# Performance work log

Measured on AMD Instinct MI355X. Metric: run time of the kernel, lower is better.

## Reference

```python
import jax, jax.numpy as jnp
import numpy as np

B, C, H, W = 4, 512, 64, 64
C8 = C // 8


def setup_inputs() -> dict:
    key = jax.random.key(0)
    ks = jax.random.split(key, 8)
    return {
        "x": jax.random.normal(ks[0], (B, C, H, W), jnp.float32),
        "wb": jax.random.normal(ks[1], (C8, C), jnp.float32) * 0.05,
        "bb": jax.random.normal(ks[2], (C8,), jnp.float32) * 0.05,
        "wc": jax.random.normal(ks[3], (C8, C), jnp.float32) * 0.05,
        "bc": jax.random.normal(ks[4], (C8,), jnp.float32) * 0.05,
        "wd": jax.random.normal(ks[5], (C, C), jnp.float32) * 0.05,
        "bd": jax.random.normal(ks[6], (C,), jnp.float32) * 0.05,
        "alpha": jax.random.normal(ks[7], (1,), jnp.float32),
    }


def reference(x, wb, bb, wc, bc, wd, bd, alpha):
    b, c, h, w = x.shape
    n = h * w
    xf = x.reshape(b, c, n)  # [B, C, N]
    # 1x1 convs == per-pixel channel matmuls
    feat_b = jnp.einsum('kc,bcn->bkn', wb, xf) + bb[:, None]  # [B, C/8, N]
    feat_c = jnp.einsum('kc,bcn->bkn', wc, xf) + bc[:, None]  # [B, C/8, N]
    # attention_s[n, m] = softmax_m( feat_b[:, n] . feat_c[:, m] )  (no scaling, as in source)
    scores = jnp.einsum('bkn,bkm->bnm', feat_b, feat_c)  # [B, N, N]
    attn = jax.nn.softmax(scores, axis=-1)
    feat_d = jnp.einsum('oc,bcn->bon', wd, xf) + bd[:, None]  # [B, C, N]
    # feat_e = bmm(feat_d, attn^T): fe[c, n] = sum_m fd[c, m] * attn[n, m]
    feat_e = jnp.einsum('bcm,bnm->bcn', feat_d, attn).reshape(b, c, h, w)
    return alpha[0] * feat_e + x
```

## Files before the change

### kernel.cpp

```cpp
#include <hip/hip_runtime.h>
#include <hip/hip_bf16.h>

#define NB 4
#define CC 512
#define CK 64
#define NN 4096

typedef unsigned short u16;
typedef __attribute__((ext_vector_type(8))) __bf16 bf16x8;
typedef __attribute__((ext_vector_type(4))) float f32x4;
typedef __attribute__((ext_vector_type(4))) unsigned int u32x4;
typedef __attribute__((ext_vector_type(8))) unsigned short u16x8;
typedef __attribute__((ext_vector_type(4))) unsigned short u16x4;

__device__ __forceinline__ u16 f2b(float f) {
  union { float f; unsigned u; } x; x.f = f;
  unsigned r = x.u + 0x7fffu + ((x.u >> 16) & 1u);
  return (u16)(r >> 16);
}
__device__ __forceinline__ float b2f(u16 u) {
  union { unsigned u; float f; } x; x.u = ((unsigned)u) << 16; return x.f;
}

#define MFMA16(a, b, c) __builtin_amdgcn_mfma_f32_16x16x32_bf16((a), (b), (c), 0, 0, 0)

__global__ __launch_bounds__(256) void proj_qk(
    const float* __restrict__ x,
    const float* __restrict__ wb, const float* __restrict__ bb,
    const float* __restrict__ wc, const float* __restrict__ bc,
    u16* __restrict__ Qhi, u16* __restrict__ Qlo,
    u16* __restrict__ Khi, u16* __restrict__ Klo)
{
  const int tid = threadIdx.x;
  const int n0 = blockIdx.x * 64;
  const int which = blockIdx.y;
  const int b = blockIdx.z;
  const float* w   = which ? wc : wb;
  const float* bia = which ? bc : bb;
  u16* oh = which ? Khi : Qhi;
  u16* ol = which ? Klo : Qlo;

  __shared__ u16 Wh[64][40], Wl[64][40], Xh[64][40], Xl[64][40];

  const int lane = tid & 63, wid = tid >> 6;
  const int wr = wid >> 1, wn = wid & 1;
  const int l15 = lane & 15, lk = (lane >> 4) * 8;

  f32x4 acc[2][2] = {};

  for (int kk = 0; kk < CC; kk += 32) {
    {
      const int row = tid >> 2, c0 = (tid & 3) * 8;
      const float* src = w + (size_t)row * CC + kk + c0;
#pragma unroll
      for (int i = 0; i < 8; ++i) {
        float v = src[i];
        u16 h = f2b(v);
        Wh[row][c0 + i] = h;
        Wl[row][c0 + i] = f2b(v - b2f(h));
      }
    }
    {
      const int cc2 = tid >> 3, j0 = (tid & 7) * 8;
      const float* src = x + ((size_t)b * CC + kk + cc2) * NN + n0 + j0;
#pragma unroll
      for (int i = 0; i < 8; ++i) {
        float v = src[i];
        u16 h = f2b(v);
        Xh[j0 + i][cc2] = h;
        Xl[j0 + i][cc2] = f2b(v - b2f(h));
      }
    }
    __syncthreads();
#pragma unroll
    for (int fi = 0; fi < 2; ++fi) {
      const int ar = wr * 32 + fi * 16 + l15;
      bf16x8 ah = *(const bf16x8*)&Wh[ar][lk];
      bf16x8 al = *(const bf16x8*)&Wl[ar][lk];
#pragma unroll
      for (int fj = 0; fj < 2; ++fj) {
        const int br = wn * 32 + fj * 16 + l15;
        bf16x8 bh = *(const bf16x8*)&Xh[br][lk];
        bf16x8 bl = *(const bf16x8*)&Xl[br][lk];
        acc[fi][fj] = MFMA16(ah, bh, acc[fi][fj]);
        acc[fi][fj] = MFMA16(ah, bl, acc[fi][fj]);
        acc[fi][fj] = MFMA16(al, bh, acc[fi][fj]);
      }
    }
    __syncthreads();
  }

#pragma unroll
  for (int fi = 0; fi < 2; ++fi) {
    const int d0 = wr * 32 + fi * 16 + (lane >> 4) * 4;
#pragma unroll
    for (int fj = 0; fj < 2; ++fj) {
      const int n = n0 + wn * 32 + fj * 16 + l15;
      u16x4 vh, vl;
#pragma unroll
      for (int r = 0; r < 4; ++r) {
        float v = acc[fi][fj][r] + bia[d0 + r];
        u16 h = f2b(v);
        vh[r] = h;
        vl[r] = f2b(v - b2f(h));
      }
      *(u16x4*)&oh[((size_t)b * NN + n) * CK + d0] = vh;
      *(u16x4*)&ol[((size_t)b * NN + n) * CK + d0] = vl;
    }
  }
}

__global__ __launch_bounds__(256) void proj_v(
    const float* __restrict__ x,
    const float* __restrict__ wd, const float* __restrict__ bd,
    u16* __restrict__ Vt)
{
  const int tid = threadIdx.x;
  const int n0 = blockIdx.x * 64;
  const int o0 = blockIdx.y * 64;
  const int b = blockIdx.z;

  __shared__ u16 Wt[64][40], Xt[64][40];
  const int lane = tid & 63, wid = tid >> 6;
  const int wr = wid >> 1, wn = wid & 1;
  const int l15 = lane & 15, lk = (lane >> 4) * 8;

  f32x4 acc[2][2] = {};
  for (int kk = 0; kk < CC; kk += 32) {
    {
      const int row = tid >> 2, c0 = (tid & 3) * 8;
      const float* src = wd + (size_t)(o0 + row) * CC + kk + c0;
#pragma unroll
      for (int i = 0; i < 8; ++i) Wt[row][c0 + i] = f2b(src[i]);
    }
    {
      const int cc2 = tid >> 3, j0 = (tid & 7) * 8;
      const float* src = x + ((size_t)b * CC + kk + cc2) * NN + n0 + j0;
#pragma unroll
      for (int i = 0; i < 8; ++i) Xt[j0 + i][cc2] = f2b(src[i]);
    }
    __syncthreads();
#pragma unroll
    for (int fi = 0; fi < 2; ++fi) {
      bf16x8 a = *(const bf16x8*)&Wt[wr * 32 + fi * 16 + l15][lk];
#pragma unroll
      for (int fj = 0; fj < 2; ++fj) {
        bf16x8 bv = *(const bf16x8*)&Xt[wn * 32 + fj * 16 + l15][lk];
        acc[fi][fj] = MFMA16(a, bv, acc[fi][fj]);
      }
    }
    __syncthreads();
  }
#pragma unroll
  for (int fi = 0; fi < 2; ++fi) {
    const int d0 = o0 + wr * 32 + fi * 16 + (lane >> 4) * 4;
#pragma unroll
    for (int fj = 0; fj < 2; ++fj) {
      const int n = n0 + wn * 32 + fj * 16 + l15;
#pragma unroll
      for (int r = 0; r < 4; ++r)
        Vt[((size_t)b * CC + d0 + r) * NN + n] = f2b(acc[fi][fj][r] + bd[d0 + r]);
    }
  }
}

struct alignas(16) AttnLds {
  u16 kh[2][64][64];
  u16 kl[2][64][64];
  float s[64][68];
  u16 p[64][64];
  float m[64];
  float l[64];
  float sc[64];
};

__global__ __launch_bounds__(256, 2) void attn(
    const u16* __restrict__ Qhi, const u16* __restrict__ Qlo,
    const u16* __restrict__ Khi, const u16* __restrict__ Klo,
    const u16* __restrict__ Vt,
    const float* __restrict__ x, const float* __restrict__ alpha,
    float* __restrict__ out)
{
  __shared__ AttnLds L;
  const int tid = threadIdx.x;
  const int lane = tid & 63, wid = tid >> 6;
  const int bid = blockIdx.x;
  const int b = (bid >> 1) & 3;
  const int qt = bid >> 3;
  const int ohalf = bid & 1;
  const int q0 = qt * 64;
  const int l15 = lane & 15;
  const int lk8 = (lane >> 4) * 8;

  const int srow = tid >> 2;
  const int sch  = (tid & 3) * 16;
  const int ssw0 = sch ^ ((srow & 7) << 3);
  const int ssw1 = (sch + 8) ^ ((srow & 7) << 3);

  bf16x8 qah[2], qal[2];
  {
    const size_t qg = ((size_t)b * NN + q0 + wid * 16 + l15) * CK + lk8;
    qah[0] = *(const bf16x8*)&Qhi[qg];
    qah[1] = *(const bf16x8*)&Qhi[qg + 32];
    qal[0] = *(const bf16x8*)&Qlo[qg];
    qal[1] = *(const bf16x8*)&Qlo[qg + 32];
  }
  {
    const size_t g = ((size_t)b * NN + srow) * CK + sch;
    *(u32x4*)&L.kh[0][srow][ssw0] = *(const u32x4*)&Khi[g];
    *(u32x4*)&L.kh[0][srow][ssw1] = *(const u32x4*)&Khi[g + 8];
    *(u32x4*)&L.kl[0][srow][ssw0] = *(const u32x4*)&Klo[g];
    *(u32x4*)&L.kl[0][srow][ssw1] = *(const u32x4*)&Klo[g + 8];
  }
  if (tid < 64) { L.m[tid] = -__builtin_huge_valf(); L.l[tid] = 0.f; }

  const u16* vbase = Vt + ((size_t)b * CC + ohalf * 256 + wid * 64 + l15) * NN + lk8;

  f32x4 accO[4][4] = {};

  __syncthreads();

  for (int t = 0; t < 64; ++t) {
    const int m0 = t * 64;
    const int cur = t & 1;
    const bool hasNext = (t < 63);

    u32x4 kh0, kh1, kl0, kl1;
    if (hasNext) {
      const size_t g = ((size_t)b * NN + m0 + 64 + srow) * CK + sch;
      kh0 = *(const u32x4*)&Khi[g];
      kh1 = *(const u32x4*)&Khi[g + 8];
      kl0 = *(const u32x4*)&Klo[g];
      kl1 = *(const u32x4*)&Klo[g + 8];
    }
    bf16x8 vr[2][4];
#pragma unroll
    for (int f_ = 0; f_ < 4; ++f_)
#pragma unroll
      for (int ks = 0; ks < 2; ++ks)
        vr[ks][f_] = *(const bf16x8*)(vbase + (size_t)f_ * 16 * NN + m0 + ks * 32);

    __builtin_amdgcn_s_setprio(1);
#pragma unroll
    for (int fj = 0; fj < 4; ++fj) {
      f32x4 s = {};
#pragma unroll
      for (int ks = 0; ks < 2; ++ks) {
        const int k = ks * 32 + lk8;
        const int br = fj * 16 + l15;
        bf16x8 bh = *(const bf16x8*)&L.kh[cur][br][k ^ ((br & 7) << 3)];
        bf16x8 bl = *(const bf16x8*)&L.kl[cur][br][k ^ ((br & 7) << 3)];
        s = MFMA16(qah[ks], bh, s);
        s = MFMA16(qah[ks], bl, s);
        s = MFMA16(qal[ks], bh, s);
      }
      const int r0 = wid * 16 + (lane >> 4) * 4, c0 = fj * 16 + l15;
#pragma unroll
      for (int r = 0; r < 4; ++r) L.s[r0 + r][c0] = s[r];
    }
    __builtin_amdgcn_s_setprio(0);
    __syncthreads();

    if (hasNext) {
      *(u32x4*)&L.kh[cur ^ 1][srow][ssw0] = kh0;
      *(u32x4*)&L.kh[cur ^ 1][srow][ssw1] = kh1;
      *(u32x4*)&L.kl[cur ^ 1][srow][ssw0] = kl0;
      *(u32x4*)&L.kl[cur ^ 1][srow][ssw1] = kl1;
    }
    {
      const int row = srow, sub = tid & 3;
      const float* sr = &L.s[row][sch];
      f32x4 a0 = *(const f32x4*)&sr[0];
      f32x4 a1 = *(const f32x4*)&sr[4];
      f32x4 a2 = *(const f32x4*)&sr[8];
      f32x4 a3 = *(const f32x4*)&sr[12];
      float mx = fmaxf(fmaxf(fmaxf(a0[0], a0[1]), fmaxf(a0[2], a0[3])),
                       fmaxf(fmaxf(a1[0], a1[1]), fmaxf(a1[2], a1[3])));
      mx = fmaxf(mx, fmaxf(fmaxf(fmaxf(a2[0], a2[1]), fmaxf(a2[2], a2[3])),
                           fmaxf(fmaxf(a3[0], a3[1]), fmaxf(a3[2], a3[3]))));
      mx = fmaxf(mx, __shfl_xor(mx, 1));
      mx = fmaxf(mx, __shfl_xor(mx, 2));
      const float mOld = L.m[row];
      const float mNew = fmaxf(mOld, mx);
      float pv[16];
      float sum = 0.f;
#pragma unroll
      for (int j = 0; j < 4; ++j) { pv[j]      = __expf(a0[j] - mNew); sum += pv[j]; }
#pragma unroll
      for (int j = 0; j < 4; ++j) { pv[4 + j]  = __expf(a1[j] - mNew); sum += pv[4 + j]; }
#pragma unroll
      for (int j = 0; j < 4; ++j) { pv[8 + j]  = __expf(a2[j] - mNew); sum += pv[8 + j]; }
#pragma unroll
      for (int j = 0; j < 4; ++j) { pv[12 + j] = __expf(a3[j] - mNew); sum += pv[12 + j]; }
      sum += __shfl_xor(sum, 1);
      sum += __shfl_xor(sum, 2);
      const float scf = __expf(mOld - mNew);
      if (sub == 0) {
        L.m[row] = mNew;
        L.l[row] = L.l[row] * scf + sum;
        L.sc[row] = scf;
      }
      u16x8 pb0, pb1;
#pragma unroll
      for (int j = 0; j < 8; ++j) pb0[j] = f2b(pv[j]);
#pragma unroll
      for (int j = 0; j < 8; ++j) pb1[j] = f2b(pv[8 + j]);
      *(u16x8*)&L.p[row][ssw0] = pb0;
      *(u16x8*)&L.p[row][ssw1] = pb1;
    }
    __syncthreads();

#pragma unroll
    for (int f_ = 0; f_ < 4; ++f_) {
      const int r0 = f_ * 16 + (lane >> 4) * 4;
      float s0 = L.sc[r0], s1 = L.sc[r0 + 1], s2 = L.sc[r0 + 2], s3 = L.sc[r0 + 3];
#pragma unroll
      for (int fj = 0; fj < 4; ++fj) {
        accO[f_][fj][0] *= s0; accO[f_][fj][1] *= s1;
        accO[f_][fj][2] *= s2; accO[f_][fj][3] *= s3;
      }
    }
    __builtin_amdgcn_s_setprio(1);
#pragma unroll
    for (int ks = 0; ks < 2; ++ks) {
      const int k = ks * 32 + lk8;
      bf16x8 a[4];
#pragma unroll
      for (int f_ = 0; f_ < 4; ++f_) {
        const int ar = f_ * 16 + l15;
        a[f_] = *(const bf16x8*)&L.p[ar][k ^ ((ar & 7) << 3)];
      }
#pragma unroll
      for (int fj = 0; fj < 4; ++fj)
#pragma unroll
        for (int f_ = 0; f_ < 4; ++f_)
          accO[f_][fj] = MFMA16(a[f_], vr[ks][fj], accO[f_][fj]);
    }
    __builtin_amdgcn_s_setprio(0);
  }
  __syncthreads();
  const float al = alpha[0];
#pragma unroll
  for (int f_ = 0; f_ < 4; ++f_) {
    const int r0 = f_ * 16 + (lane >> 4) * 4;
    const float rl0 = 1.f / L.l[r0],     rl1 = 1.f / L.l[r0 + 1];
    const float rl2 = 1.f / L.l[r0 + 2], rl3 = 1.f / L.l[r0 + 3];
    const int n_ = q0 + r0;
#pragma unroll
    for (int fj = 0; fj < 4; ++fj) {
      const int c_ = ohalf * 256 + wid * 64 + fj * 16 + l15;
      const size_t g = ((size_t)b * CC + c_) * NN + n_;
      f32x4 xv = *(const f32x4*)&x[g];
      f32x4 ov;
      ov[0] = fmaf(al, accO[f_][fj][0] * rl0, xv[0]);
      ov[1] = fmaf(al, accO[f_][fj][1] * rl1, xv[1]);
      ov[2] = fmaf(al, accO[f_][fj][2] * rl2, xv[2]);
      ov[3] = fmaf(al, accO[f_][fj][3] * rl3, xv[3]);
      *(f32x4*)&out[g] = ov;
    }
  }
}

extern "C" void kernel_launch(void* const* d_in, const int* in_sizes, int n_in,
                              void* d_out, int out_size, void* d_ws, size_t ws_size,
                              hipStream_t stream) {
  const float* x     = (const float*)d_in[0];
  const float* wb    = (const float*)d_in[1];
  const float* bb    = (const float*)d_in[2];
  const float* wc    = (const float*)d_in[3];
  const float* bc    = (const float*)d_in[4];
  const float* wd    = (const float*)d_in[5];
  const float* bd    = (const float*)d_in[6];
  const float* alpha = (const float*)d_in[7];
  float* out = (float*)d_out;

  u16* Qhi = (u16*)d_ws;
  u16* Qlo = Qhi + (size_t)NB * NN * CK;
  u16* Khi = Qlo + (size_t)NB * NN * CK;
  u16* Klo = Khi + (size_t)NB * NN * CK;
  u16* Vt  = Klo + (size_t)NB * NN * CK;

  proj_qk<<<dim3(NN / 64, 2, NB), 256, 0, stream>>>(x, wb, bb, wc, bc, Qhi, Qlo, Khi, Klo);
  proj_v<<<dim3(NN / 64, CC / 64, NB), 256, 0, stream>>>(x, wd, bd, Vt);
  attn<<<dim3(512), 256, 0, stream>>>(Qhi, Qlo, Khi, Klo, Vt, x, alpha, out);
}
```

Before: 233.8 us.

## Retile attention to 32-query blocks covering all channels, with exp2 and lazy rescale

The attention kernel now gives each block 32 queries and all 512 output channels, instead of 64 queries and half the channels. This stops recomputing QK scores and softmax twice per query tile, at the cost of streaming all of V for each block. Q is pre-scaled by log2(e) in the projection so the softmax can use exp2f. The running max is only raised when it grows by more than a threshold, and the accumulator rescale is skipped when no row changed. The rescale threshold allows unnormalized exponents up to about 2^11.5, which risks precision loss in bf16 P, and the V loads are split around the score computation.

New measurement: 346.7 us. +48.3%, slower.

```diff
diff --git a/kernel.cpp b/kernel.cpp
--- a/kernel.cpp
+++ b/kernel.cpp
@@ -20,6 +20,9 @@
 }
 __device__ __forceinline__ float b2f(u16 u) {
   union { unsigned u; float f; } x; x.u = ((unsigned)u) << 16; return x.f;
+}
+__device__ __forceinline__ u16 cvt_bf16(float f) {
+  union { __bf16 h; u16 u; } c; c.h = (__bf16)f; return c.u;
 }
 
 #define MFMA16(a, b, c) __builtin_amdgcn_mfma_f32_16x16x32_bf16((a), (b), (c), 0, 0, 0)
@@ -39,6 +42,7 @@
   const float* bia = which ? bc : bb;
   u16* oh = which ? Khi : Qhi;
   u16* ol = which ? Klo : Qlo;
+  const float qsc = which ? 1.0f : 1.44269504088896340736f;
 
   __shared__ u16 Wh[64][40], Wl[64][40], Xh[64][40], Xl[64][40];
 
@@ -99,7 +103,7 @@
       u16x4 vh, vl;
 #pragma unroll
       for (int r = 0; r < 4; ++r) {
-        float v = acc[fi][fj][r] + bia[d0 + r];
+        float v = (acc[fi][fj][r] + bia[d0 + r]) * qsc;
         u16 h = f2b(v);
         vh[r] = h;
         vl[r] = f2b(v - b2f(h));
@@ -167,11 +171,11 @@
 struct alignas(16) AttnLds {
   u16 kh[2][64][64];
   u16 kl[2][64][64];
-  float s[64][68];
-  u16 p[64][64];
-  float m[64];
-  float l[64];
-  float sc[64];
+  float s[32][68];
+  u16 p[32][64];
+  float m[32];
+  float l[32];
+  float sc[32];
 };
 
 __global__ __launch_bounds__(256, 2) void attn(
@@ -186,20 +190,25 @@
   const int lane = tid & 63, wid = tid >> 6;
   const int bid = blockIdx.x;
   const int b = (bid >> 1) & 3;
-  const int qt = bid >> 3;
-  const int ohalf = bid & 1;
-  const int q0 = qt * 64;
+  const int qt = ((bid >> 3) << 1) | (bid & 1);
+  const int q0 = qt * 32;
   const int l15 = lane & 15;
   const int lk8 = (lane >> 4) * 8;
+
+  const int fi = wid >> 1;
+  const int fj0 = (wid & 1) * 2;
 
   const int srow = tid >> 2;
   const int sch  = (tid & 3) * 16;
   const int ssw0 = sch ^ ((srow & 7) << 3);
   const int ssw1 = (sch + 8) ^ ((srow & 7) << 3);
 
+  const int xrow = tid >> 3, xsub = tid & 7;
+  const int xsw = (xsub * 8) ^ ((xrow & 7) << 3);
+
   bf16x8 qah[2], qal[2];
   {
-    const size_t qg = ((size_t)b * NN + q0 + wid * 16 + l15) * CK + lk8;
+    const size_t qg = ((size_t)b * NN + q0 + fi * 16 + l15) * CK + lk8;
     qah[0] = *(const bf16x8*)&Qhi[qg];
     qah[1] = *(const bf16x8*)&Qhi[qg + 32];
     qal[0] = *(const bf16x8*)&Qlo[qg];
@@ -212,11 +221,11 @@
     *(u32x4*)&L.kl[0][srow][ssw0] = *(const u32x4*)&Klo[g];
     *(u32x4*)&L.kl[0][srow][ssw1] = *(const u32x4*)&Klo[g + 8];
   }
-  if (tid < 64) { L.m[tid] = -__builtin_huge_valf(); L.l[tid] = 0.f; }
-
-  const u16* vbase = Vt + ((size_t)b * CC + ohalf * 256 + wid * 64 + l15) * NN + lk8;
-
-  f32x4 accO[4][4] = {};
+  if (tid < 32) { L.m[tid] = -__builtin_huge_valf(); L.l[tid] = 0.f; }
+
+  const u16* vbase = Vt + ((size_t)b * CC + wid * 128 + l15) * NN + lk8;
+
+  f32x4 accO[2][8] = {};
 
   __syncthreads();
 
@@ -233,16 +242,15 @@
       kl0 = *(const u32x4*)&Klo[g];
       kl1 = *(const u32x4*)&Klo[g + 8];
     }
-    bf16x8 vr[2][4];
-#pragma unroll
-    for (int f_ = 0; f_ < 4; ++f_)
-#pragma unroll
-      for (int ks = 0; ks < 2; ++ks)
-        vr[ks][f_] = *(const bf16x8*)(vbase + (size_t)f_ * 16 * NN + m0 + ks * 32);
+    bf16x8 vr0[8], vr1[8];
+#pragma unroll
+    for (int f_ = 0; f_ < 8; ++f_)
+      vr0[f_] = *(const bf16x8*)(vbase + (size_t)f_ * 16 * NN + m0);
 
     __builtin_amdgcn_s_setprio(1);
 #pragma unroll
-    for (int fj = 0; fj < 4; ++fj) {
+    for (int f2 = 0; f2 < 2; ++f2) {
+      const int fj = fj0 + f2;
       f32x4 s = {};
 #pragma unroll
       for (int ks = 0; ks < 2; ++ks) {
@@ -254,11 +262,15 @@
         s = MFMA16(qah[ks], bl, s);
         s = MFMA16(qal[ks], bh, s);
       }
-      const int r0 = wid * 16 + (lane >> 4) * 4, c0 = fj * 16 + l15;
+      const int r0 = fi * 16 + (lane >> 4) * 4, c0 = fj * 16 + l15;
 #pragma unroll
       for (int r = 0; r < 4; ++r) L.s[r0 + r][c0] = s[r];
     }
     __builtin_amdgcn_s_setprio(0);
+#pragma unroll
+    for (int f_ = 0; f_ < 8; ++f_)
+      vr1[f_] = *(const bf16x8*)(vbase + (size_t)f_ * 16 * NN + m0 + 32);
+
     __syncthreads();
 
     if (hasNext) {
@@ -268,87 +280,91 @@
       *(u32x4*)&L.kl[cur ^ 1][srow][ssw1] = kl1;
     }
     {
-      const int row = srow, sub = tid & 3;
-      const float* sr = &L.s[row][sch];
+      const float* sr = &L.s[xrow][xsub * 8];
       f32x4 a0 = *(const f32x4*)&sr[0];
       f32x4 a1 = *(const f32x4*)&sr[4];
-      f32x4 a2 = *(const f32x4*)&sr[8];
-      f32x4 a3 = *(const f32x4*)&sr[12];
       float mx = fmaxf(fmaxf(fmaxf(a0[0], a0[1]), fmaxf(a0[2], a0[3])),
                        fmaxf(fmaxf(a1[0], a1[1]), fmaxf(a1[2], a1[3])));
-      mx = fmaxf(mx, fmaxf(fmaxf(fmaxf(a2[0], a2[1]), fmaxf(a2[2], a2[3])),
-                           fmaxf(fmaxf(a3[0], a3[1]), fmaxf(a3[2], a3[3]))));
       mx = fmaxf(mx, __shfl_xor(mx, 1));
       mx = fmaxf(mx, __shfl_xor(mx, 2));
-      const float mOld = L.m[row];
-      const float mNew = fmaxf(mOld, mx);
-      float pv[16];
-      float sum = 0.f;
-#pragma unroll
-      for (int j = 0; j < 4; ++j) { pv[j]      = __expf(a0[j] - mNew); sum += pv[j]; }
-#pragma unroll
-      for (int j = 0; j < 4; ++j) { pv[4 + j]  = __expf(a1[j] - mNew); sum += pv[4 + j]; }
-#pragma unroll
-      for (int j = 0; j < 4; ++j) { pv[8 + j]  = __expf(a2[j] - mNew); sum += pv[8 + j]; }
-#pragma unroll
-      for (int j = 0; j < 4; ++j) { pv[12 + j] = __expf(a3[j] - mNew); sum += pv[12 + j]; }
+      mx = fmaxf(mx, __shfl_xor(mx, 4));
+      const float mOld = L.m[xrow];
+      const bool grow = (mx > mOld + 11.5f);
+      const float mNew = grow ? mx : mOld;
+      float pv[8], sum = 0.f;
+#pragma unroll
+      for (int j = 0; j < 4; ++j) { pv[j] = exp2f(a0[j] - mNew); sum += pv[j]; }
+#pragma unroll
+      for (int j = 0; j < 4; ++j) { pv[4 + j] = exp2f(a1[j] - mNew); sum += pv[4 + j]; }
       sum += __shfl_xor(sum, 1);
       sum += __shfl_xor(sum, 2);
-      const float scf = __expf(mOld - mNew);
-      if (sub == 0) {
-        L.m[row] = mNew;
-        L.l[row] = L.l[row] * scf + sum;
-        L.sc[row] = scf;
-      }
-      u16x8 pb0, pb1;
-#pragma unroll
-      for (int j = 0; j < 8; ++j) pb0[j] = f2b(pv[j]);
-#pragma unroll
-      for (int j = 0; j < 8; ++j) pb1[j] = f2b(pv[8 + j]);
-      *(u16x8*)&L.p[row][ssw0] = pb0;
-      *(u16x8*)&L.p[row][ssw1] = pb1;
-    }
-    __syncthreads();
-
-#pragma unroll
-    for (int f_ = 0; f_ < 4; ++f_) {
-      const int r0 = f_ * 16 + (lane >> 4) * 4;
-      float s0 = L.sc[r0], s1 = L.sc[r0 + 1], s2 = L.sc[r0 + 2], s3 = L.sc[r0 + 3];
-#pragma unroll
-      for (int fj = 0; fj < 4; ++fj) {
-        accO[f_][fj][0] *= s0; accO[f_][fj][1] *= s1;
-        accO[f_][fj][2] *= s2; accO[f_][fj][3] *= s3;
+      sum += __shfl_xor(sum, 4);
+      const float scf = grow ? exp2f(mOld - mNew) : 1.0f;
+      if (xsub == 0) {
+        if (grow) L.m[xrow] = mNew;
+        L.l[xrow] = L.l[xrow] * scf + sum;
+        L.sc[xrow] = scf;
+      }
+      u16x8 pb;
+#pragma unroll
+      for (int j = 0; j < 8; ++j) pb[j] = cvt_bf16(pv[j]);
+      *(u16x8*)&L.p[xrow][xsw] = pb;
+    }
+    __syncthreads();
+
+    {
+      float scv[8];
+      bool need = false;
+#pragma unroll
+      for (int f_ = 0; f_ < 2; ++f_)
+#pragma unroll
+        for (int r = 0; r < 4; ++r) {
+          float s_ = L.sc[f_ * 16 + (lane >> 4) * 4 + r];
+          scv[f_ * 4 + r] = s_;
+          need |= (s_ != 1.0f);
+        }
+      if (__any(need)) {
+#pragma unroll
+        for (int f_ = 0; f_ < 2; ++f_)
+#pragma unroll
+          for (int fj = 0; fj < 8; ++fj)
+#pragma unroll
+            for (int r = 0; r < 4; ++r)
+              accO[f_][fj][r] *= scv[f_ * 4 + r];
       }
     }
     __builtin_amdgcn_s_setprio(1);
-#pragma unroll
-    for (int ks = 0; ks < 2; ++ks) {
-      const int k = ks * 32 + lk8;
-      bf16x8 a[4];
-#pragma unroll
-      for (int f_ = 0; f_ < 4; ++f_) {
-        const int ar = f_ * 16 + l15;
-        a[f_] = *(const bf16x8*)&L.p[ar][k ^ ((ar & 7) << 3)];
-      }
-#pragma unroll
-      for (int fj = 0; fj < 4; ++fj)
-#pragma unroll
-        for (int f_ = 0; f_ < 4; ++f_)
-          accO[f_][fj] = MFMA16(a[f_], vr[ks][fj], accO[f_][fj]);
+    {
+      const int k0 = lk8;
+      bf16x8 a0 = *(const bf16x8*)&L.p[l15][k0 ^ ((l15 & 7) << 3)];
+      bf16x8 a1 = *(const bf16x8*)&L.p[16 + l15][k0 ^ ((l15 & 7) << 3)];
+#pragma unroll
+      for (int fj = 0; fj < 8; ++fj) {
+        accO[0][fj] = MFMA16(a0, vr0[fj], accO[0][fj]);
+        accO[1][fj] = MFMA16(a1, vr0[fj], accO[1][fj]);
+      }
+      const int k1 = 32 + lk8;
+      bf16x8 a2 = *(const bf16x8*)&L.p[l15][k1 ^ ((l15 & 7) << 3)];
+      bf16x8 a3 = *(const bf16x8*)&L.p[16 + l15][k1 ^ ((l15 & 7) << 3)];
+#pragma unroll
+      for (int fj = 0; fj < 8; ++fj) {
+        accO[0][fj] = MFMA16(a2, vr1[fj], accO[0][fj]);
+        accO[1][fj] = MFMA16(a3, vr1[fj], accO[1][fj]);
+      }
     }
     __builtin_amdgcn_s_setprio(0);
   }
   __syncthreads();
   const float al = alpha[0];
 #pragma unroll
-  for (int f_ = 0; f_ < 4; ++f_) {
+  for (int f_ = 0; f_ < 2; ++f_) {
     const int r0 = f_ * 16 + (lane >> 4) * 4;
     const float rl0 = 1.f / L.l[r0],     rl1 = 1.f / L.l[r0 + 1];
     const float rl2 = 1.f / L.l[r0 + 2], rl3 = 1.f / L.l[r0 + 3];
     const int n_ = q0 + r0;
 #pragma unroll
-    for (int fj = 0; fj < 4; ++fj) {
-      const int c_ = ohalf * 256 + wid * 64 + fj * 16 + l15;
+    for (int fj = 0; fj < 8; ++fj) {
+      const int c_ = wid * 128 + fj * 16 + l15;
       const size_t g = ((size_t)b * CC + c_) * NN + n_;
       f32x4 xv = *(const f32x4*)&x[g];
       f32x4 ov;
```

## Use exp2 with log2e folded into Q, lazy softmax rescaling, single K buffer

Applied to the files above, without the earlier changes.

The Q projection now scales its output by log2(e), so the attention softmax can use exp2f instead of __expf. The running max is only raised when the new tile max exceeds it by a threshold. The accumulator rescale is skipped wave-wide when no row's scale factor changed. Probabilities are converted to bf16 with the native conversion instead of a manual rounding routine, and the K tile in LDS goes from double-buffered to single-buffered to cut LDS use. These aim to trim ALU work in the softmax and rescale path between MFMA phases. The cost is larger unnormalized probabilities, up to about 2^11.5, which slightly changes numerics.

Result: slower. 242.9 us (+3.9%).

```diff
diff --git a/kernel.cpp b/kernel.cpp
--- a/kernel.cpp
+++ b/kernel.cpp
@@ -20,6 +20,9 @@
 }
 __device__ __forceinline__ float b2f(u16 u) {
   union { unsigned u; float f; } x; x.u = ((unsigned)u) << 16; return x.f;
+}
+__device__ __forceinline__ u16 cvt_bf16(float f) {
+  union { __bf16 h; u16 u; } c; c.h = (__bf16)f; return c.u;
 }
 
 #define MFMA16(a, b, c) __builtin_amdgcn_mfma_f32_16x16x32_bf16((a), (b), (c), 0, 0, 0)
@@ -39,6 +42,7 @@
   const float* bia = which ? bc : bb;
   u16* oh = which ? Khi : Qhi;
   u16* ol = which ? Klo : Qlo;
+  const float qsc = which ? 1.0f : 1.44269504088896340736f;
 
   __shared__ u16 Wh[64][40], Wl[64][40], Xh[64][40], Xl[64][40];
 
@@ -99,7 +103,7 @@
       u16x4 vh, vl;
 #pragma unroll
       for (int r = 0; r < 4; ++r) {
-        float v = acc[fi][fj][r] + bia[d0 + r];
+        float v = (acc[fi][fj][r] + bia[d0 + r]) * qsc;
         u16 h = f2b(v);
         vh[r] = h;
         vl[r] = f2b(v - b2f(h));
@@ -165,8 +169,8 @@
 }
 
 struct alignas(16) AttnLds {
-  u16 kh[2][64][64];
-  u16 kl[2][64][64];
+  u16 kh[64][64];
+  u16 kl[64][64];
   float s[64][68];
   u16 p[64][64];
   float m[64];
@@ -207,10 +211,10 @@
   }
   {
     const size_t g = ((size_t)b * NN + srow) * CK + sch;
-    *(u32x4*)&L.kh[0][srow][ssw0] = *(const u32x4*)&Khi[g];
-    *(u32x4*)&L.kh[0][srow][ssw1] = *(const u32x4*)&Khi[g + 8];
-    *(u32x4*)&L.kl[0][srow][ssw0] = *(const u32x4*)&Klo[g];
-    *(u32x4*)&L.kl[0][srow][ssw1] = *(const u32x4*)&Klo[g + 8];
+    *(u32x4*)&L.kh[srow][ssw0] = *(const u32x4*)&Khi[g];
+    *(u32x4*)&L.kh[srow][ssw1] = *(const u32x4*)&Khi[g + 8];
+    *(u32x4*)&L.kl[srow][ssw0] = *(const u32x4*)&Klo[g];
+    *(u32x4*)&L.kl[srow][ssw1] = *(const u32x4*)&Klo[g + 8];
   }
   if (tid < 64) { L.m[tid] = -__builtin_huge_valf(); L.l[tid] = 0.f; }
 
@@ -222,7 +226,6 @@
 
   for (int t = 0; t < 64; ++t) {
     const int m0 = t * 64;
-    const int cur = t & 1;
     const bool hasNext = (t < 63);
 
     u32x4 kh0, kh1, kl0, kl1;
@@ -248,8 +251,8 @@
       for (int ks = 0; ks < 2; ++ks) {
         const int k = ks * 32 + lk8;
         const int br = fj * 16 + l15;
-        bf16x8 bh = *(const bf16x8*)&L.kh[cur][br][k ^ ((br & 7) << 3)];
-        bf16x8 bl = *(const bf16x8*)&L.kl[cur][br][k ^ ((br & 7) << 3)];
+        bf16x8 bh = *(const bf16x8*)&L.kh[br][k ^ ((br & 7) << 3)];
+        bf16x8 bl = *(const bf16x8*)&L.kl[br][k ^ ((br & 7) << 3)];
         s = MFMA16(qah[ks], bh, s);
         s = MFMA16(qah[ks], bl, s);
         s = MFMA16(qal[ks], bh, s);
@@ -262,10 +265,10 @@
     __syncthreads();
 
     if (hasNext) {
-      *(u32x4*)&L.kh[cur ^ 1][srow][ssw0] = kh0;
-      *(u32x4*)&L.kh[cur ^ 1][srow][ssw1] = kh1;
-      *(u32x4*)&L.kl[cur ^ 1][srow][ssw0] = kl0;
-      *(u32x4*)&L.kl[cur ^ 1][srow][ssw1] = kl1;
+      *(u32x4*)&L.kh[srow][ssw0] = kh0;
+      *(u32x4*)&L.kh[srow][ssw1] = kh1;
+      *(u32x4*)&L.kl[srow][ssw0] = kl0;
+      *(u32x4*)&L.kl[srow][ssw1] = kl1;
     }
     {
       const int row = srow, sub = tid & 3;
@@ -281,43 +284,53 @@
       mx = fmaxf(mx, __shfl_xor(mx, 1));
       mx = fmaxf(mx, __shfl_xor(mx, 2));
       const float mOld = L.m[row];
-      const float mNew = fmaxf(mOld, mx);
+      const bool grow = (mx > mOld + 11.5f);
+      const float mNew = grow ? mx : mOld;
       float pv[16];
       float sum = 0.f;
 #pragma unroll
-      for (int j = 0; j < 4; ++j) { pv[j]      = __expf(a0[j] - mNew); sum += pv[j]; }
-#pragma unroll
-      for (int j = 0; j < 4; ++j) { pv[4 + j]  = __expf(a1[j] - mNew); sum += pv[4 + j]; }
-#pragma unroll
-      for (int j = 0; j < 4; ++j) { pv[8 + j]  = __expf(a2[j] - mNew); sum += pv[8 + j]; }
-#pragma unroll
-      for (int j = 0; j < 4; ++j) { pv[12 + j] = __expf(a3[j] - mNew); sum += pv[12 + j]; }
+      for (int j = 0; j < 4; ++j) { pv[j]      = exp2f(a0[j] - mNew); sum += pv[j]; }
+#pragma unroll
+      for (int j = 0; j < 4; ++j) { pv[4 + j]  = exp2f(a1[j] - mNew); sum += pv[4 + j]; }
+#pragma unroll
+      for (int j = 0; j < 4; ++j) { pv[8 + j]  = exp2f(a2[j] - mNew); sum += pv[8 + j]; }
+#pragma unroll
+      for (int j = 0; j < 4; ++j) { pv[12 + j] = exp2f(a3[j] - mNew); sum += pv[12 + j]; }
       sum += __shfl_xor(sum, 1);
       sum += __shfl_xor(sum, 2);
-      const float scf = __expf(mOld - mNew);
+      const float scf = grow ? exp2f(mOld - mNew) : 1.0f;
       if (sub == 0) {
-        L.m[row] = mNew;
+        if (grow) L.m[row] = mNew;
         L.l[row] = L.l[row] * scf + sum;
         L.sc[row] = scf;
       }
       u16x8 pb0, pb1;
 #pragma unroll
-      for (int j = 0; j < 8; ++j) pb0[j] = f2b(pv[j]);
-#pragma unroll
-      for (int j = 0; j < 8; ++j) pb1[j] = f2b(pv[8 + j]);
+      for (int j = 0; j < 8; ++j) pb0[j] = cvt_bf16(pv[j]);
+#pragma unroll
+      for (int j = 0; j < 8; ++j) pb1[j] = cvt_bf16(pv[8 + j]);
       *(u16x8*)&L.p[row][ssw0] = pb0;
       *(u16x8*)&L.p[row][ssw1] = pb1;
     }
     __syncthreads();
 
-#pragma unroll
-    for (int f_ = 0; f_ < 4; ++f_) {
-      const int r0 = f_ * 16 + (lane >> 4) * 4;
-      float s0 = L.sc[r0], s1 = L.sc[r0 + 1], s2 = L.sc[r0 + 2], s3 = L.sc[r0 + 3];
-#pragma unroll
-      for (int fj = 0; fj < 4; ++fj) {
-        accO[f_][fj][0] *= s0; accO[f_][fj][1] *= s1;
-        accO[f_][fj][2] *= s2; accO[f_][fj][3] *= s3;
+    {
+      f32x4 scv[4];
+      bool need = false;
+#pragma unroll
+      for (int f_ = 0; f_ < 4; ++f_) {
+        scv[f_] = *(const f32x4*)&L.sc[f_ * 16 + (lane >> 4) * 4];
+        need |= (scv[f_][0] != 1.0f) | (scv[f_][1] != 1.0f) |
+                (scv[f_][2] != 1.0f) | (scv[f_][3] != 1.0f);
+      }
+      if (__any(need)) {
+#pragma unroll
+        for (int f_ = 0; f_ < 4; ++f_)
+#pragma unroll
+          for (int fj = 0; fj < 4; ++fj)
+#pragma unroll
+            for (int r = 0; r < 4; ++r)
+              accO[f_][fj][r] *= scv[f_][r];
       }
     }
     __builtin_amdgcn_s_setprio(1);
```
